# Kernel optimization log

Hardware: AMD Instinct MI355X
Metric: run time of the kernel (lower is better)

The kernel has to match this reference:

```python
import jax, jax.numpy as jnp
import numpy as np
from jax import lax

B_, L_, D_ = 4, 2048, 256
DI, NS, DC, DTR = 512, 16, 4, 16  # d_inner=2*D, d_state, d_conv, dt_rank=ceil(D/16)
DFF = 4 * D_


def setup_inputs():
    key = jax.random.key(0)
    ks = jax.random.split(key, 20)
    rn = lambda k, s, sc=0.02: jax.random.normal(k, s, jnp.float32) * sc
    return {
        "x": jax.random.normal(ks[0], (B_, L_, D_), jnp.float32),
        "in_proj_w": rn(ks[1], (2 * DI, D_)), "in_proj_b": jnp.zeros((2 * DI,), jnp.float32),
        "conv_w": rn(ks[2], (DI, DC), 0.1), "conv_b": jnp.zeros((DI,), jnp.float32),
        "x_proj_w": rn(ks[3], (DTR + 2 * NS, DI)),
        "dt_proj_w": rn(ks[4], (DI, DTR), 0.1), "dt_proj_b": rn(ks[5], (DI,), 0.5),
        "A_log": jnp.log(jnp.tile(jnp.arange(1, NS + 1, dtype=jnp.float32), (DI, 1))),
        "D_ssm": jnp.ones((DI,), jnp.float32),
        "out_proj_w": rn(ks[6], (D_, DI)), "out_proj_b": jnp.zeros((D_,), jnp.float32),
        "ln1_g": jnp.ones((D_,), jnp.float32), "ln1_b": jnp.zeros((D_,), jnp.float32),
        "fc1_w": rn(ks[7], (DFF, D_)), "fc1_b": jnp.zeros((DFF,), jnp.float32),
        "fc2_w": rn(ks[8], (D_, DFF)), "fc2_b": jnp.zeros((D_,), jnp.float32),
        "ln2_g": jnp.ones((D_,), jnp.float32), "ln2_b": jnp.zeros((D_,), jnp.float32),
    }


def _layer_norm(x, g, b, eps=1e-5):
    m = jnp.mean(x, -1, keepdims=True)
    v = jnp.mean((x - m) ** 2, -1, keepdims=True)
    return (x - m) / jnp.sqrt(v + eps) * g + b


def _mamba(x, in_proj_w, in_proj_b, conv_w, conv_b, x_proj_w, dt_proj_w, dt_proj_b, A_log, D_ssm, out_proj_w, out_proj_b):
    B, L, D = x.shape
    xz = x @ in_proj_w.T + in_proj_b                       # [B,L,2*DI]
    xi, z = jnp.split(xz, 2, axis=-1)
    # causal depthwise conv over time
    xc = jnp.transpose(xi, (0, 2, 1))                       # [B,DI,L]
    xc = lax.conv_general_dilated(xc, conv_w[:, None, :], (1,), [(DC - 1, 0)],
                                  dimension_numbers=("NCH", "OIH", "NCH"),
                                  feature_group_count=DI)
    xi = jax.nn.silu(jnp.transpose(xc + conv_b[None, :, None], (0, 2, 1)))  # [B,L,DI]
    x_dbl = xi @ x_proj_w.T                                 # [B,L,DTR+2*NS]
    dt, Bs, Cs = jnp.split(x_dbl, [DTR, DTR + NS], axis=-1)
    dt = jax.nn.softplus(dt @ dt_proj_w.T + dt_proj_b)      # [B,L,DI]
    A = -jnp.exp(A_log)                                     # [DI,NS]
    dA = jnp.exp(dt[..., None] * A)                         # [B,L,DI,NS]
    dBu = dt[..., None] * Bs[:, :, None, :] * xi[..., None]  # [B,L,DI,NS]
    dA_t = jnp.moveaxis(dA, 1, 0)
    dBu_t = jnp.moveaxis(dBu, 1, 0)
    C_t = jnp.moveaxis(Cs, 1, 0)                            # [L,B,NS]

    def step(h, inp):
        a, bu, c = inp
        h = a * h + bu                                      # [B,DI,NS]
        y = jnp.einsum("bdn,bn->bd", h, c)
        return h, y

    h0 = jnp.zeros((B, DI, NS), x.dtype)
    _, ys = lax.scan(step, h0, (dA_t, dBu_t, C_t))
    y = jnp.moveaxis(ys, 0, 1) + xi * D_ssm                 # [B,L,DI]
    y = y * jax.nn.silu(z)
    return y @ out_proj_w.T + out_proj_b


def reference(x, in_proj_w, in_proj_b, conv_w, conv_b, x_proj_w, dt_proj_w, dt_proj_b,
              A_log, D_ssm, out_proj_w, out_proj_b, ln1_g, ln1_b, fc1_w, fc1_b,
              fc2_w, fc2_b, ln2_g, ln2_b):
    gelu = lambda t: jax.nn.gelu(t, approximate=False)
    ssm = _mamba(x, in_proj_w, in_proj_b, conv_w, conv_b, x_proj_w, dt_proj_w,
                 dt_proj_b, A_log, D_ssm, out_proj_w, out_proj_b)
    y = _layer_norm(x + ssm, ln1_g, ln1_b)                  # dropout = identity (eval)
    ffn = gelu(gelu(y @ fc1_w.T + fc1_b) @ fc2_w.T + fc2_b)
    return _layer_norm(y + ffn, ln2_g, ln2_b)
```

## Files before the change

### kernel.cpp

```cpp
#include <hip/hip_runtime.h>

typedef __bf16 bf16x8 __attribute__((ext_vector_type(8)));
typedef float  f32x4  __attribute__((ext_vector_type(4)));

#define AS1 __attribute__((address_space(1)))
#define AS3 __attribute__((address_space(3)))

__device__ __forceinline__ float bf2f(ushort u) {
    union { unsigned int i; float f; } v; v.i = ((unsigned int)u) << 16; return v.f;
}
__device__ __forceinline__ ushort f2bf(float f) {
    union { float f; unsigned int i; } v; v.f = f;
    unsigned int i = v.i;
    unsigned int r = i + 0x7FFFu + ((i >> 16) & 1u);
    return (ushort)(r >> 16);
}
__device__ __forceinline__ float bflo(unsigned int u) { return bf2f((ushort)(u & 0xFFFFu)); }
__device__ __forceinline__ float bfhi(unsigned int u) { return bf2f((ushort)(u >> 16)); }
__device__ __forceinline__ float gelu_f(float v) {
    return 0.5f * v * (1.f + erff(v * 0.70710678118654752f));
}

__device__ __forceinline__ bool sniff_inline(const ushort* __restrict__ x) {
    const int lane = threadIdx.x & 63;
    int cnt = 0;
    #pragma unroll
    for (int r = 0; r < 4; r++) {
        const ushort u = x[lane + r * 64];
        const int e = (u >> 7) & 0xFF;
        if ((u & 0x7FFF) == 0 || (e >= 112 && e <= 141)) cnt++;
    }
    #pragma unroll
    for (int o = 32; o > 0; o >>= 1) cnt += __shfl_xor(cnt, o);
    return cnt >= 224;
}

struct CanonArgs {
    const void* src[20];
    int off[20];
    int total;
};

__launch_bounds__(256)
__global__ void canon_k(CanonArgs a, ushort* __restrict__ dst, ushort* __restrict__ xpw_pad,
                        const ushort* __restrict__ sniffx)
{
    const int i = blockIdx.x * 256 + threadIdx.x;
    if (i >= a.total) {
        const int j = i - a.total;
        if (j < 8192) xpw_pad[24576 + j] = 0;
        return;
    }
    const bool fl = sniff_inline(sniffx);
    int s = 0;
    #pragma unroll
    for (int t = 1; t < 20; t++) if (i >= a.off[t]) s = t;
    const int li = i - a.off[s];
    ushort v;
    if (fl) v = ((const ushort*)a.src[s])[li];
    else    v = f2bf(((const float*)a.src[s])[li]);
    dst[i] = v;
    if (s == 5) xpw_pad[li] = v;
}

template<int BM, int BN>
__launch_bounds__(256, 2)
__global__ void gemm_bt(const ushort* __restrict__ A, const ushort* __restrict__ W,
                        const ushort* __restrict__ bias, ushort* __restrict__ Cb,
                        int N, int K)
{
    constexpr int WMT = BM / 32;
    constexpr int WNT = BN / 32;
    __shared__ __align__(16) ushort As[BM * 32];
    __shared__ __align__(16) ushort Bs[BN * 32];
    const int tid  = threadIdx.x;
    const int wave = tid >> 6;
    const int lane = tid & 63;
    const int m0 = blockIdx.x * BM;
    const int n0 = blockIdx.y * BN;
    const int wm = (wave >> 1) * (BM / 2);
    const int wn = (wave & 1) * (BN / 2);
    const int lrow = lane & 15;
    const int quad = lane >> 4;

    f32x4 acc[WMT][WNT];
    #pragma unroll
    for (int i = 0; i < WMT; i++)
        #pragma unroll
        for (int j = 0; j < WNT; j++)
            #pragma unroll
            for (int r = 0; r < 4; r++) acc[i][j][r] = 0.f;

    for (int k0 = 0; k0 < K; k0 += 32) {
        #pragma unroll
        for (int t = 0; t < BM / 64; t++) {
            const int inst = t * 4 + wave;
            const int row  = inst * 16 + (lane >> 2);
            const int sub  = lane & 3;
            const ushort* gp = A + (size_t)(m0 + row) * K + (k0 + sub * 8);
            __builtin_amdgcn_global_load_lds((AS1 void*)(void*)gp,
                                             (AS3 void*)(As + inst * 512), 16, 0, 0);
        }
        #pragma unroll
        for (int t = 0; t < BN / 64; t++) {
            const int inst = t * 4 + wave;
            const int row  = inst * 16 + (lane >> 2);
            const int sub  = lane & 3;
            const ushort* gp = W + (size_t)(n0 + row) * K + (k0 + sub * 8);
            __builtin_amdgcn_global_load_lds((AS1 void*)(void*)gp,
                                             (AS3 void*)(Bs + inst * 512), 16, 0, 0);
        }
        __syncthreads();
        bf16x8 afr[WMT], bfr[WNT];
        #pragma unroll
        for (int i = 0; i < WMT; i++)
            afr[i] = *(const bf16x8*)&As[(wm + i * 16 + lrow) * 32 + quad * 8];
        #pragma unroll
        for (int j = 0; j < WNT; j++)
            bfr[j] = *(const bf16x8*)&Bs[(wn + j * 16 + lrow) * 32 + quad * 8];
        #pragma unroll
        for (int i = 0; i < WMT; i++)
            #pragma unroll
            for (int j = 0; j < WNT; j++)
                acc[i][j] = __builtin_amdgcn_mfma_f32_16x16x32_bf16(afr[i], bfr[j], acc[i][j], 0, 0, 0);
        __syncthreads();
    }

    #pragma unroll
    for (int i = 0; i < WMT; i++) {
        const int gm = m0 + wm + i * 16 + quad * 4;
        #pragma unroll
        for (int j = 0; j < WNT; j++) {
            const int gn = n0 + wn + j * 16 + lrow;
            const float bv = bf2f(bias[gn]);
            #pragma unroll
            for (int r = 0; r < 4; r++)
                Cb[(size_t)(gm + r) * N + gn] = f2bf(acc[i][j][r] + bv);
        }
    }
}

__launch_bounds__(512)
__global__ void convx_k(const ushort* __restrict__ xz, const ushort* __restrict__ cw,
                        const ushort* __restrict__ cb, const ushort* __restrict__ xpw_pad,
                        ushort* __restrict__ xc, float* __restrict__ xdbl)
{
    __shared__ __align__(16) ushort xcs[16 * 520];
    const int tid  = threadIdx.x;
    const int wave = tid >> 6;
    const int lane = tid & 63;
    const int lrow = lane & 15;
    const int quad = lane >> 4;
    const int c = blockIdx.x, b = blockIdx.y;
    const int t0 = b * 2048 + c * 16;

    {
        const int d8 = (tid & 63) * 8;
        ushort wl[32];
        *(uint4*)&wl[0]  = *(const uint4*)&cw[d8 * 4];
        *(uint4*)&wl[8]  = *(const uint4*)&cw[d8 * 4 + 8];
        *(uint4*)&wl[16] = *(const uint4*)&cw[d8 * 4 + 16];
        *(uint4*)&wl[24] = *(const uint4*)&cw[d8 * 4 + 24];
        ushort bl[8];
        *(uint4*)&bl[0] = *(const uint4*)&cb[d8];
        #pragma unroll
        for (int it = 0; it < 2; it++) {
            const int trow = it * 8 + wave;
            const int t = t0 + trow;
            const int l = t & 2047;
            float acc[8];
            #pragma unroll
            for (int j = 0; j < 8; j++) acc[j] = bf2f(bl[j]);
            #pragma unroll
            for (int k = 0; k < 4; k++) {
                const int ls = l - 3 + k;
                if (ls >= 0) {
                    ushort xl[8];
                    *(uint4*)&xl[0] = *(const uint4*)&xz[(size_t)(t - 3 + k) * 1024 + d8];
                    #pragma unroll
                    for (int j = 0; j < 8; j++) acc[j] += bf2f(xl[j]) * bf2f(wl[j * 4 + k]);
                }
            }
            ushort ol[8];
            #pragma unroll
            for (int j = 0; j < 8; j++) {
                const float s = acc[j] / (1.f + __expf(-acc[j]));
                ol[j] = f2bf(s);
            }
            *(uint4*)&xcs[trow * 520 + d8] = *(uint4*)&ol[0];
        }
    }
    __syncthreads();

    if (wave < 3) {
        const int nt = wave;
        const ushort* bptr = xpw_pad + (size_t)(nt * 16 + lrow) * 512 + quad * 8;
        f32x4 acc = {0.f, 0.f, 0.f, 0.f};
        #pragma unroll
        for (int hh = 0; hh < 2; hh++) {
            bf16x8 Bv[8];
            #pragma unroll
            for (int s = 0; s < 8; s++)
                Bv[s] = *(const bf16x8*)(bptr + hh * 256 + s * 32);
            #pragma unroll
            for (int s = 0; s < 8; s++) {
                const bf16x8 afr = *(const bf16x8*)&xcs[lrow * 520 + hh * 256 + s * 32 + quad * 8];
                acc = __builtin_amdgcn_mfma_f32_16x16x32_bf16(afr, Bv[s], acc, 0, 0, 0);
            }
        }
        const int col = nt * 16 + lrow;
        if (col < 48) {
            #pragma unroll
            for (int r = 0; r < 4; r++)
                xdbl[(size_t)(t0 + quad * 4 + r) * 64 + col] = acc[r];
        }
    }

    {
        const int row = tid >> 5;
        const int col = (tid & 31) * 16;
        *(uint4*)&xc[(size_t)(t0 + row) * 512 + col]     = *(const uint4*)&xcs[row * 520 + col];
        *(uint4*)&xc[(size_t)(t0 + row) * 512 + col + 8] = *(const uint4*)&xcs[row * 520 + col + 8];
    }
}

__launch_bounds__(256)
__global__ void scan1_k(const ushort* __restrict__ xc, const float* __restrict__ xdbl,
                        const ushort* __restrict__ dtw, const ushort* __restrict__ dtb,
                        const ushort* __restrict__ Alog,
                        float* __restrict__ summh, float* __restrict__ sdtb)
{
    __shared__ float XD[16 * 48];
    const int tid = threadIdx.x;
    const int c = blockIdx.x, dh = blockIdx.y, b = blockIdx.z;
    const int t0 = b * 2048 + c * 16;
    const int d = dh * 256 + tid;

    for (int e = tid; e < 768; e += 256)
        XD[e] = xdbl[(size_t)(t0 + (e / 48)) * 64 + (e % 48)];
    __syncthreads();

    const uint4 w0 = *(const uint4*)&dtw[d * 16];
    const uint4 w1 = *(const uint4*)&dtw[d * 16 + 8];
    const float wd[16] = { bflo(w0.x), bfhi(w0.x), bflo(w0.y), bfhi(w0.y),
                           bflo(w0.z), bfhi(w0.z), bflo(w0.w), bfhi(w0.w),
                           bflo(w1.x), bfhi(w1.x), bflo(w1.y), bfhi(w1.y),
                           bflo(w1.z), bfhi(w1.z), bflo(w1.w), bfhi(w1.w) };
    const uint4 a0 = *(const uint4*)&Alog[d * 16];
    const uint4 a1 = *(const uint4*)&Alog[d * 16 + 8];
    const float al[16] = { bflo(a0.x), bfhi(a0.x), bflo(a0.y), bfhi(a0.y),
                           bflo(a0.z), bfhi(a0.z), bflo(a0.w), bfhi(a0.w),
                           bflo(a1.x), bfhi(a1.x), bflo(a1.y), bfhi(a1.y),
                           bflo(a1.z), bfhi(a1.z), bflo(a1.w), bfhi(a1.w) };
    const float dtbv = bf2f(dtb[d]);
    float A[16], h[16];
    #pragma unroll
    for (int n = 0; n < 16; n++) { A[n] = -__expf(al[n]); h[n] = 0.f; }
    float sdt = 0.f;
    for (int i = 0; i < 16; i++) {
        const float* Xr = &XD[i * 48];
        float s0 = dtbv, s1 = 0.f, s2 = 0.f, s3 = 0.f;
        #pragma unroll
        for (int k = 0; k < 16; k += 4) {
            s0 += Xr[k]     * wd[k];
            s1 += Xr[k + 1] * wd[k + 1];
            s2 += Xr[k + 2] * wd[k + 2];
            s3 += Xr[k + 3] * wd[k + 3];
        }
        const float s = (s0 + s1) + (s2 + s3);
        const float dtv = (s > 15.f) ? s : __logf(1.f + __expf(s));
        const float xiv = bf2f(xc[(size_t)(t0 + i) * 512 + d]);
        const float dx = dtv * xiv;
        sdt += dtv;
        #pragma unroll
        for (int n = 0; n < 16; n++) {
            const float da = __expf(dtv * A[n]);
            h[n] = da * h[n] + dx * Xr[16 + n];
        }
    }
    const size_t bh = ((size_t)(b * 128 + c) * 16) * 512 + d;
    #pragma unroll
    for (int n = 0; n < 16; n++) summh[bh + (size_t)n * 512] = h[n];
    sdtb[(size_t)(b * 128 + c) * 512 + d] = sdt;
}

__launch_bounds__(128)
__global__ void combine_k(float* __restrict__ summh, const float* __restrict__ sdtb,
                          const ushort* __restrict__ Alog)
{
    const int b  = blockIdx.x >> 6;
    const int n  = (blockIdx.x >> 2) & 15;
    const int dq = blockIdx.x & 3;
    const int d  = dq * 128 + threadIdx.x;
    const float An = -__expf(bf2f(Alog[d * 16 + n]));
    float h = 0.f;
    #pragma unroll
    for (int q = 0; q < 4; q++) {
        float p[32], hl[32], ho[32];
        #pragma unroll
        for (int c2 = 0; c2 < 32; c2++) {
            const int cc = q * 32 + c2;
            hl[c2] = summh[((size_t)(b * 128 + cc) * 16 + n) * 512 + d];
            p[c2]  = __expf(An * sdtb[(size_t)(b * 128 + cc) * 512 + d]);
        }
        #pragma unroll
        for (int c2 = 0; c2 < 32; c2++) {
            ho[c2] = h;
            h = p[c2] * h + hl[c2];
        }
        #pragma unroll
        for (int c2 = 0; c2 < 32; c2++)
            summh[((size_t)(b * 128 + (q * 32 + c2)) * 16 + n) * 512 + d] = ho[c2];
    }
}

__launch_bounds__(256)
__global__ void scan2_k(ushort* __restrict__ xz, const ushort* __restrict__ xc,
                        const float* __restrict__ xdbl,
                        const ushort* __restrict__ dtw, const ushort* __restrict__ dtb,
                        const ushort* __restrict__ Alog, const float* __restrict__ summh,
                        const ushort* __restrict__ Dssm)
{
    __shared__ float XD[16 * 48];
    const int tid = threadIdx.x;
    const int c = blockIdx.x, dh = blockIdx.y, b = blockIdx.z;
    const int t0 = b * 2048 + c * 16;
    const int d = dh * 256 + tid;

    for (int e = tid; e < 768; e += 256)
        XD[e] = xdbl[(size_t)(t0 + (e / 48)) * 64 + (e % 48)];
    __syncthreads();

    const uint4 w0 = *(const uint4*)&dtw[d * 16];
    const uint4 w1 = *(const uint4*)&dtw[d * 16 + 8];
    const float wd[16] = { bflo(w0.x), bfhi(w0.x), bflo(w0.y), bfhi(w0.y),
                           bflo(w0.z), bfhi(w0.z), bflo(w0.w), bfhi(w0.w),
                           bflo(w1.x), bfhi(w1.x), bflo(w1.y), bfhi(w1.y),
                           bflo(w1.z), bfhi(w1.z), bflo(w1.w), bfhi(w1.w) };
    const uint4 a0 = *(const uint4*)&Alog[d * 16];
    const uint4 a1 = *(const uint4*)&Alog[d * 16 + 8];
    const float al[16] = { bflo(a0.x), bfhi(a0.x), bflo(a0.y), bfhi(a0.y),
                           bflo(a0.z), bfhi(a0.z), bflo(a0.w), bfhi(a0.w),
                           bflo(a1.x), bfhi(a1.x), bflo(a1.y), bfhi(a1.y),
                           bflo(a1.z), bfhi(a1.z), bflo(a1.w), bfhi(a1.w) };
    const float dtbv = bf2f(dtb[d]);
    float A[16], h[16];
    #pragma unroll
    for (int n = 0; n < 16; n++) A[n] = -__expf(al[n]);
    const size_t bh = ((size_t)(b * 128 + c) * 16) * 512 + d;
    #pragma unroll
    for (int n = 0; n < 16; n++) h[n] = summh[bh + (size_t)n * 512];
    const float Dv = bf2f(Dssm[d]);

    for (int i = 0; i < 16; i++) {
        const int t = t0 + i;
        const float* Xr = &XD[i * 48];
        float s0 = dtbv, s1 = 0.f, s2 = 0.f, s3 = 0.f;
        #pragma unroll
        for (int k = 0; k < 16; k += 4) {
            s0 += Xr[k]     * wd[k];
            s1 += Xr[k + 1] * wd[k + 1];
            s2 += Xr[k + 2] * wd[k + 2];
            s3 += Xr[k + 3] * wd[k + 3];
        }
        const float s = (s0 + s1) + (s2 + s3);
        const float dtv = (s > 15.f) ? s : __logf(1.f + __expf(s));
        const float xiv = bf2f(xc[(size_t)t * 512 + d]);
        const float dx = dtv * xiv;
        float yv0 = 0.f, yv1 = 0.f;
        #pragma unroll
        for (int n = 0; n < 16; n += 2) {
            const float da0 = __expf(dtv * A[n]);
            const float da1 = __expf(dtv * A[n + 1]);
            h[n]     = da0 * h[n]     + dx * Xr[16 + n];
            h[n + 1] = da1 * h[n + 1] + dx * Xr[17 + n];
            yv0 += h[n]     * Xr[32 + n];
            yv1 += h[n + 1] * Xr[33 + n];
        }
        float yv = yv0 + yv1;
        yv += xiv * Dv;
        const float zv = bf2f(xz[(size_t)t * 1024 + 512 + d]);
        yv *= zv / (1.f + __expf(-zv));
        xz[(size_t)t * 1024 + d] = f2bf(yv);
    }
}

__launch_bounds__(512, 4)
__global__ void ffn_k(const ushort* __restrict__ xz, const ushort* __restrict__ cx,
                      const ushort* __restrict__ opw, const ushort* __restrict__ opb,
                      const ushort* __restrict__ ln1g, const ushort* __restrict__ ln1b,
                      const ushort* __restrict__ f1w, const ushort* __restrict__ f1b,
                      const ushort* __restrict__ f2w, const ushort* __restrict__ f2b,
                      const ushort* __restrict__ ln2g, const ushort* __restrict__ ln2b,
                      void* __restrict__ dout, const ushort* __restrict__ sniffx)
{
    __shared__ __align__(16) ushort yls[16 * 520];
    __shared__ __align__(16) ushort y1bs[16 * 264];
    __shared__ float redS[8 * 16], redQ[8 * 16];
    ushort* f1q = yls;

    const int tid  = threadIdx.x;
    const int wave = tid >> 6;
    const int lane = tid & 63;
    const int lrow = lane & 15;
    const int quad = lane >> 4;
    const int c = blockIdx.x, b = blockIdx.y;
    const int t0 = b * 2048 + c * 16;
    const int n0w = wave * 32;

    {
        const int row = tid >> 5;
        const int col = (tid & 31) * 16;
        *(uint4*)&yls[row * 520 + col]     = *(const uint4*)&xz[(size_t)(t0 + row) * 1024 + col];
        *(uint4*)&yls[row * 520 + col + 8] = *(const uint4*)&xz[(size_t)(t0 + row) * 1024 + col + 8];
    }
    __syncthreads();

    f32x4 accP[2];
    #pragma unroll
    for (int j = 0; j < 2; j++)
        #pragma unroll
        for (int r = 0; r < 4; r++) accP[j][r] = 0.f;
    {
        const ushort* bp0 = opw + (size_t)(n0w + lrow) * 512 + quad * 8;
        const ushort* bp1 = opw + (size_t)(n0w + 16 + lrow) * 512 + quad * 8;
        #pragma unroll
        for (int hh = 0; hh < 2; hh++) {
            bf16x8 B0[8], B1[8];
            #pragma unroll
            for (int s = 0; s < 8; s++) {
                B0[s] = *(const bf16x8*)(bp0 + hh * 256 + s * 32);
                B1[s] = *(const bf16x8*)(bp1 + hh * 256 + s * 32);
            }
            #pragma unroll
            for (int s = 0; s < 8; s++) {
                const bf16x8 afr = *(const bf16x8*)&yls[lrow * 520 + hh * 256 + s * 32 + quad * 8];
                accP[0] = __builtin_amdgcn_mfma_f32_16x16x32_bf16(afr, B0[s], accP[0], 0, 0, 0);
                accP[1] = __builtin_amdgcn_mfma_f32_16x16x32_bf16(afr, B1[s], accP[1], 0, 0, 0);
            }
        }
    }
    float vP[2][4];
    float ps[4], pq[4];
    #pragma unroll
    for (int r = 0; r < 4; r++) { ps[r] = 0.f; pq[r] = 0.f; }
    #pragma unroll
    for (int j = 0; j < 2; j++) {
        const int col = n0w + j * 16 + lrow;
        const float bv = bf2f(opb[col]);
        #pragma unroll
        for (int r = 0; r < 4; r++) {
            const int row = quad * 4 + r;
            float v = accP[j][r] + bv + bf2f(cx[(size_t)(t0 + row) * 256 + col]);
            vP[j][r] = v;
            ps[r] += v;
            pq[r] += v * v;
        }
    }
    #pragma unroll
    for (int r = 0; r < 4; r++) {
        #pragma unroll
        for (int o = 8; o > 0; o >>= 1) {
            ps[r] += __shfl_xor(ps[r], o);
            pq[r] += __shfl_xor(pq[r], o);
        }
        if (lrow == 0) {
            const int row = quad * 4 + r;
            redS[wave * 16 + row] = ps[r];
            redQ[wave * 16 + row] = pq[r];
        }
    }
    __syncthreads();

    float y1f[2][4];
    #pragma unroll
    for (int r = 0; r < 4; r++) {
        const int row = quad * 4 + r;
        float S = 0.f, Q = 0.f;
        #pragma unroll
        for (int w = 0; w < 8; w++) { S += redS[w * 16 + row]; Q += redQ[w * 16 + row]; }
        const float mean = S * (1.f / 256.f);
        const float var  = Q * (1.f / 256.f) - mean * mean;
        const float rs   = rsqrtf(var + 1e-5f);
        #pragma unroll
        for (int j = 0; j < 2; j++) {
            const int col = n0w + j * 16 + lrow;
            const float o2 = (vP[j][r] - mean) * rs * bf2f(ln1g[col]) + bf2f(ln1b[col]);
            y1f[j][r] = o2;
            y1bs[row * 264 + col] = f2bf(o2);
        }
    }
    __syncthreads();

    f32x4 acc2[2];
    #pragma unroll
    for (int j = 0; j < 2; j++)
        #pragma unroll
        for (int r = 0; r < 4; r++) acc2[j][r] = 0.f;

    for (int q = 0; q < 4; q++) {
        f32x4 a1[2];
        #pragma unroll
        for (int j = 0; j < 2; j++)
            #pragma unroll
            for (int r = 0; r < 4; r++) a1[j][r] = 0.f;
        {
            const ushort* bp0 = f1w + (size_t)(q * 256 + n0w + lrow) * 256 + quad * 8;
            const ushort* bp1 = f1w + (size_t)(q * 256 + n0w + 16 + lrow) * 256 + quad * 8;
            bf16x8 B0[8], B1[8];
            #pragma unroll
            for (int s = 0; s < 8; s++) {
                B0[s] = *(const bf16x8*)(bp0 + s * 32);
                B1[s] = *(const bf16x8*)(bp1 + s * 32);
            }
            #pragma unroll
            for (int s = 0; s < 8; s++) {
                const bf16x8 afr = *(const bf16x8*)&y1bs[lrow * 264 + s * 32 + quad * 8];
                a1[0] = __builtin_amdgcn_mfma_f32_16x16x32_bf16(afr, B0[s], a1[0], 0, 0, 0);
                a1[1] = __builtin_amdgcn_mfma_f32_16x16x32_bf16(afr, B1[s], a1[1], 0, 0, 0);
            }
        }
        #pragma unroll
        for (int j = 0; j < 2; j++) {
            const int qc = n0w + j * 16 + lrow;
            const float bv = bf2f(f1b[q * 256 + qc]);
            #pragma unroll
            for (int r = 0; r < 4; r++) {
                const int row = quad * 4 + r;
                f1q[row * 260 + qc] = f2bf(gelu_f(a1[j][r] + bv));
            }
        }
        __syncthreads();
        {
            const ushort* bp0 = f2w + (size_t)(n0w + lrow) * 1024 + q * 256 + quad * 8;
            const ushort* bp1 = f2w + (size_t)(n0w + 16 + lrow) * 1024 + q * 256 + quad * 8;
            bf16x8 B0[8], B1[8];
            #pragma unroll
            for (int s = 0; s < 8; s++) {
                B0[s] = *(const bf16x8*)(bp0 + s * 32);
                B1[s] = *(const bf16x8*)(bp1 + s * 32);
            }
            #pragma unroll
            for (int s = 0; s < 8; s++) {
                const bf16x8 afr = *(const bf16x8*)&f1q[lrow * 260 + s * 32 + quad * 8];
                acc2[0] = __builtin_amdgcn_mfma_f32_16x16x32_bf16(afr, B0[s], acc2[0], 0, 0, 0);
                acc2[1] = __builtin_amdgcn_mfma_f32_16x16x32_bf16(afr, B1[s], acc2[1], 0, 0, 0);
            }
        }
        __syncthreads();
    }

    float v2[2][4];
    #pragma unroll
    for (int r = 0; r < 4; r++) { ps[r] = 0.f; pq[r] = 0.f; }
    #pragma unroll
    for (int j = 0; j < 2; j++) {
        const int col = n0w + j * 16 + lrow;
        const float bv = bf2f(f2b[col]);
        #pragma unroll
        for (int r = 0; r < 4; r++) {
            const float v = gelu_f(acc2[j][r] + bv) + y1f[j][r];
            v2[j][r] = v;
            ps[r] += v;
            pq[r] += v * v;
        }
    }
    #pragma unroll
    for (int r = 0; r < 4; r++) {
        #pragma unroll
        for (int o = 8; o > 0; o >>= 1) {
            ps[r] += __shfl_xor(ps[r], o);
            pq[r] += __shfl_xor(pq[r], o);
        }
        if (lrow == 0) {
            const int row = quad * 4 + r;
            redS[wave * 16 + row] = ps[r];
            redQ[wave * 16 + row] = pq[r];
        }
    }
    __syncthreads();

    const bool fl = sniff_inline(sniffx);
    #pragma unroll
    for (int r = 0; r < 4; r++) {
        const int row = quad * 4 + r;
        float S = 0.f, Q = 0.f;
        #pragma unroll
        for (int w = 0; w < 8; w++) { S += redS[w * 16 + row]; Q += redQ[w * 16 + row]; }
        const float mean = S * (1.f / 256.f);
        const float var  = Q * (1.f / 256.f) - mean * mean;
        const float rs   = rsqrtf(var + 1e-5f);
        #pragma unroll
        for (int j = 0; j < 2; j++) {
            const int col = n0w + j * 16 + lrow;
            const size_t off = (size_t)(t0 + row) * 256 + col;
            const float o2 = (v2[j][r] - mean) * rs * bf2f(ln2g[col]) + bf2f(ln2b[col]);
            if (fl) ((ushort*)dout)[off] = f2bf(o2);
            else    ((float*)dout)[off]  = o2;
        }
    }
}

extern "C" void kernel_launch(void* const* d_in, const int* in_sizes, int n_in,
                              void* d_out, int out_size, void* d_ws, size_t ws_size,
                              hipStream_t stream)
{
    char* ws = (char*)d_ws;
    ushort* canon = (ushort*)(ws + 256);

    static const int coff[20] = {
        0,        2097152,  2359296,  2360320,  2362368,
        2362880,  2387456,  2395648,  2396160,  2404352,
        2404864,  2535936,  2536192,  2536448,  2536704,
        2798848,  2799872,  3062016,  3062272,  3062528 };
    static const int ctot = 3062784;

    CanonArgs ca;
    for (int i = 0; i < 20; i++) { ca.src[i] = d_in[i]; ca.off[i] = coff[i]; }
    ca.total = ctot;

    const ushort* cx   = canon + coff[0];
    const ushort* cipw = canon + coff[1];
    const ushort* cipb = canon + coff[2];
    const ushort* ccw  = canon + coff[3];
    const ushort* ccb  = canon + coff[4];
    const ushort* cdtw = canon + coff[6];
    const ushort* cdtb = canon + coff[7];
    const ushort* calog= canon + coff[8];
    const ushort* cdssm= canon + coff[9];
    const ushort* copw = canon + coff[10];
    const ushort* copb = canon + coff[11];
    const ushort* cln1g= canon + coff[12];
    const ushort* cln1b= canon + coff[13];
    const ushort* cf1w = canon + coff[14];
    const ushort* cf1b = canon + coff[15];
    const ushort* cf2w = canon + coff[16];
    const ushort* cf2b = canon + coff[17];
    const ushort* cln2g= canon + coff[18];
    const ushort* cln2b= canon + coff[19];

    ushort* xpw_pad = (ushort*)(ws + 6291456);
    ushort* xz      = (ushort*)(ws + 8388608);
    float*  xdbl    = (float*)(ws + 25165824);
    float*  summh   = (float*)(ws + 27262976);
    float*  sdtb    = (float*)(ws + 44040192);
    ushort* xc      = (ushort*)(ws + 45088768);
    const ushort* sx = (const ushort*)d_in[0];

    canon_k<<<(ctot + 8192 + 255) / 256, 256, 0, stream>>>(ca, canon, xpw_pad, sx);
    gemm_bt<128, 128><<<dim3(64, 8), 256, 0, stream>>>(cx, cipw, cipb, xz, 1024, 256);
    convx_k<<<dim3(128, 4), 512, 0, stream>>>(xz, ccw, ccb, xpw_pad, xc, xdbl);
    scan1_k<<<dim3(128, 2, 4), 256, 0, stream>>>(xc, xdbl, cdtw, cdtb, calog, summh, sdtb);
    combine_k<<<256, 128, 0, stream>>>(summh, sdtb, calog);
    scan2_k<<<dim3(128, 2, 4), 256, 0, stream>>>(xz, xc, xdbl, cdtw, cdtb, calog, summh, cdssm);
    ffn_k<<<dim3(128, 4), 512, 0, stream>>>(
        xz, cx, copw, copb, cln1g, cln1b, cf1w, cf1b, cf2w, cf2b, cln2g, cln2b,
        d_out, sx);
}
```

Measured before the change: 274.0 us.

## Split fused FFN kernel into tiled GEMMs with LN1 and LN2 epilogue kernels

Replaces the monolithic per-16-row ffn_k, which reloaded weights from global per block, with a 128x256 out_proj GEMM fused with residual plus LayerNorm1, two tiled LDS GEMMs for fc1 (with GELU epilogue) and fc2 (fp32 output), and a small LN2 kernel. The aim is better weight reuse and MFMA utilisation through larger tiles. The cost is extra kernel launches and global round-trips for y1, h1 and y2, plus reuse of workspace regions. scan2 now writes its output into xc instead of xz.

New measurement: 278.2 us. About the same (+1.5%).

```diff
diff --git a/kernel.cpp b/kernel.cpp
--- a/kernel.cpp
+++ b/kernel.cpp
@@ -63,10 +63,10 @@
     if (s == 5) xpw_pad[li] = v;
 }
 
-template<int BM, int BN>
+template<int BM, int BN, int EPI, bool OUTF>
 __launch_bounds__(256, 2)
-__global__ void gemm_bt(const ushort* __restrict__ A, const ushort* __restrict__ W,
-                        const ushort* __restrict__ bias, ushort* __restrict__ Cb,
+__global__ void gemm_bt(const ushort* __restrict__ A, int lda, const ushort* __restrict__ W,
+                        const ushort* __restrict__ bias, void* __restrict__ Cb,
                         int N, int K)
 {
     constexpr int WMT = BM / 32;
@@ -97,7 +97,7 @@
             const int inst = t * 4 + wave;
             const int row  = inst * 16 + (lane >> 2);
             const int sub  = lane & 3;
-            const ushort* gp = A + (size_t)(m0 + row) * K + (k0 + sub * 8);
+            const ushort* gp = A + (size_t)(m0 + row) * lda + (k0 + sub * 8);
             __builtin_amdgcn_global_load_lds((AS1 void*)(void*)gp,
                                              (AS3 void*)(As + inst * 512), 16, 0, 0);
         }
@@ -134,8 +134,130 @@
             const int gn = n0 + wn + j * 16 + lrow;
             const float bv = bf2f(bias[gn]);
             #pragma unroll
-            for (int r = 0; r < 4; r++)
-                Cb[(size_t)(gm + r) * N + gn] = f2bf(acc[i][j][r] + bv);
+            for (int r = 0; r < 4; r++) {
+                float v = acc[i][j][r] + bv;
+                if (EPI == 1) v = gelu_f(v);
+                if (OUTF) ((float*)Cb)[(size_t)(gm + r) * N + gn] = v;
+                else      ((ushort*)Cb)[(size_t)(gm + r) * N + gn] = f2bf(v);
+            }
+        }
+    }
+}
+
+__launch_bounds__(512)
+__global__ void gemmln1_k(const ushort* __restrict__ A, const ushort* __restrict__ W,
+                          const ushort* __restrict__ bias, const ushort* __restrict__ cx,
+                          const ushort* __restrict__ g1, const ushort* __restrict__ b1,
+                          ushort* __restrict__ y1b, float* __restrict__ y1f)
+{
+    __shared__ __align__(16) ushort As[128 * 32];
+    __shared__ __align__(16) ushort Bs[256 * 32];
+    __shared__ float redS[4 * 128], redQ[4 * 128];
+    const int tid  = threadIdx.x;
+    const int wave = tid >> 6;
+    const int lane = tid & 63;
+    const int lrow = lane & 15;
+    const int quad = lane >> 4;
+    const int m0 = blockIdx.x * 128;
+    const int wm = (wave >> 2) * 64;
+    const int wn = (wave & 3) * 64;
+
+    f32x4 acc[4][4];
+    #pragma unroll
+    for (int i = 0; i < 4; i++)
+        #pragma unroll
+        for (int j = 0; j < 4; j++)
+            #pragma unroll
+            for (int r = 0; r < 4; r++) acc[i][j][r] = 0.f;
+
+    for (int k0 = 0; k0 < 512; k0 += 32) {
+        {
+            const int row = wave * 16 + (lane >> 2);
+            const int sub = lane & 3;
+            const ushort* gp = A + (size_t)(m0 + row) * 512 + (k0 + sub * 8);
+            __builtin_amdgcn_global_load_lds((AS1 void*)(void*)gp,
+                                             (AS3 void*)(As + wave * 512), 16, 0, 0);
+        }
+        #pragma unroll
+        for (int t = 0; t < 2; t++) {
+            const int inst = t * 8 + wave;
+            const int row  = inst * 16 + (lane >> 2);
+            const int sub  = lane & 3;
+            const ushort* gp = W + (size_t)row * 512 + (k0 + sub * 8);
+            __builtin_amdgcn_global_load_lds((AS1 void*)(void*)gp,
+                                             (AS3 void*)(Bs + inst * 512), 16, 0, 0);
+        }
+        __syncthreads();
+        bf16x8 afr[4], bfr[4];
+        #pragma unroll
+        for (int i = 0; i < 4; i++)
+            afr[i] = *(const bf16x8*)&As[(wm + i * 16 + lrow) * 32 + quad * 8];
+        #pragma unroll
+        for (int j = 0; j < 4; j++)
+            bfr[j] = *(const bf16x8*)&Bs[(wn + j * 16 + lrow) * 32 + quad * 8];
+        #pragma unroll
+        for (int i = 0; i < 4; i++)
+            #pragma unroll
+            for (int j = 0; j < 4; j++)
+                acc[i][j] = __builtin_amdgcn_mfma_f32_16x16x32_bf16(afr[i], bfr[j], acc[i][j], 0, 0, 0);
+        __syncthreads();
+    }
+
+    #pragma unroll
+    for (int i = 0; i < 4; i++) {
+        #pragma unroll
+        for (int j = 0; j < 4; j++) {
+            const int col = wn + j * 16 + lrow;
+            const float bv = bf2f(bias[col]);
+            #pragma unroll
+            for (int r = 0; r < 4; r++) {
+                const int rowl = wm + i * 16 + quad * 4 + r;
+                acc[i][j][r] += bv + bf2f(cx[(size_t)(m0 + rowl) * 256 + col]);
+            }
+        }
+    }
+    #pragma unroll
+    for (int i = 0; i < 4; i++) {
+        #pragma unroll
+        for (int r = 0; r < 4; r++) {
+            float s = 0.f, q = 0.f;
+            #pragma unroll
+            for (int j = 0; j < 4; j++) {
+                const float v = acc[i][j][r];
+                s += v; q += v * v;
+            }
+            #pragma unroll
+            for (int o = 8; o > 0; o >>= 1) {
+                s += __shfl_xor(s, o);
+                q += __shfl_xor(q, o);
+            }
+            if (lrow == 0) {
+                const int rowl = wm + i * 16 + quad * 4 + r;
+                redS[(wave & 3) * 128 + rowl] = s;
+                redQ[(wave & 3) * 128 + rowl] = q;
+            }
+        }
+    }
+    __syncthreads();
+
+    #pragma unroll
+    for (int i = 0; i < 4; i++) {
+        #pragma unroll
+        for (int r = 0; r < 4; r++) {
+            const int rowl = wm + i * 16 + quad * 4 + r;
+            const float S = redS[rowl] + redS[128 + rowl] + redS[256 + rowl] + redS[384 + rowl];
+            const float Q = redQ[rowl] + redQ[128 + rowl] + redQ[256 + rowl] + redQ[384 + rowl];
+            const float mean = S * (1.f / 256.f);
+            const float var  = Q * (1.f / 256.f) - mean * mean;
+            const float rs   = rsqrtf(var + 1e-5f);
+            #pragma unroll
+            for (int j = 0; j < 4; j++) {
+                const int col = wn + j * 16 + lrow;
+                const float o2 = (acc[i][j][r] - mean) * rs * bf2f(g1[col]) + bf2f(b1[col]);
+                const size_t off = (size_t)(m0 + rowl) * 256 + col;
+                y1b[off] = f2bf(o2);
+                y1f[off] = o2;
+            }
         }
     }
 }
@@ -315,7 +437,7 @@
 }
 
 __launch_bounds__(256)
-__global__ void scan2_k(ushort* __restrict__ xz, const ushort* __restrict__ xc,
+__global__ void scan2_k(const ushort* __restrict__ xz, ushort* __restrict__ xc,
                         const float* __restrict__ xdbl,
                         const ushort* __restrict__ dtw, const ushort* __restrict__ dtb,
                         const ushort* __restrict__ Alog, const float* __restrict__ summh,
@@ -381,223 +503,53 @@
         yv += xiv * Dv;
         const float zv = bf2f(xz[(size_t)t * 1024 + 512 + d]);
         yv *= zv / (1.f + __expf(-zv));
-        xz[(size_t)t * 1024 + d] = f2bf(yv);
-    }
-}
-
-__launch_bounds__(512, 4)
-__global__ void ffn_k(const ushort* __restrict__ xz, const ushort* __restrict__ cx,
-                      const ushort* __restrict__ opw, const ushort* __restrict__ opb,
-                      const ushort* __restrict__ ln1g, const ushort* __restrict__ ln1b,
-                      const ushort* __restrict__ f1w, const ushort* __restrict__ f1b,
-                      const ushort* __restrict__ f2w, const ushort* __restrict__ f2b,
-                      const ushort* __restrict__ ln2g, const ushort* __restrict__ ln2b,
+        xc[(size_t)t * 512 + d] = f2bf(yv);
+    }
+}
+
+__launch_bounds__(512)
+__global__ void ln2_k(const float* __restrict__ y2, const float* __restrict__ y1f,
+                      const ushort* __restrict__ g2, const ushort* __restrict__ b2,
                       void* __restrict__ dout, const ushort* __restrict__ sniffx)
 {
-    __shared__ __align__(16) ushort yls[16 * 520];
-    __shared__ __align__(16) ushort y1bs[16 * 264];
-    __shared__ float redS[8 * 16], redQ[8 * 16];
-    ushort* f1q = yls;
-
     const int tid  = threadIdx.x;
     const int wave = tid >> 6;
     const int lane = tid & 63;
-    const int lrow = lane & 15;
-    const int quad = lane >> 4;
-    const int c = blockIdx.x, b = blockIdx.y;
-    const int t0 = b * 2048 + c * 16;
-    const int n0w = wave * 32;
-
-    {
-        const int row = tid >> 5;
-        const int col = (tid & 31) * 16;
-        *(uint4*)&yls[row * 520 + col]     = *(const uint4*)&xz[(size_t)(t0 + row) * 1024 + col];
-        *(uint4*)&yls[row * 520 + col + 8] = *(const uint4*)&xz[(size_t)(t0 + row) * 1024 + col + 8];
-    }
-    __syncthreads();
-
-    f32x4 accP[2];
-    #pragma unroll
-    for (int j = 0; j < 2; j++)
-        #pragma unroll
-        for (int r = 0; r < 4; r++) accP[j][r] = 0.f;
-    {
-        const ushort* bp0 = opw + (size_t)(n0w + lrow) * 512 + quad * 8;
-        const ushort* bp1 = opw + (size_t)(n0w + 16 + lrow) * 512 + quad * 8;
-        #pragma unroll
-        for (int hh = 0; hh < 2; hh++) {
-            bf16x8 B0[8], B1[8];
-            #pragma unroll
-            for (int s = 0; s < 8; s++) {
-                B0[s] = *(const bf16x8*)(bp0 + hh * 256 + s * 32);
-                B1[s] = *(const bf16x8*)(bp1 + hh * 256 + s * 32);
-            }
-            #pragma unroll
-            for (int s = 0; s < 8; s++) {
-                const bf16x8 afr = *(const bf16x8*)&yls[lrow * 520 + hh * 256 + s * 32 + quad * 8];
-                accP[0] = __builtin_amdgcn_mfma_f32_16x16x32_bf16(afr, B0[s], accP[0], 0, 0, 0);
-                accP[1] = __builtin_amdgcn_mfma_f32_16x16x32_bf16(afr, B1[s], accP[1], 0, 0, 0);
-            }
-        }
-    }
-    float vP[2][4];
-    float ps[4], pq[4];
-    #pragma unroll
-    for (int r = 0; r < 4; r++) { ps[r] = 0.f; pq[r] = 0.f; }
-    #pragma unroll
-    for (int j = 0; j < 2; j++) {
-        const int col = n0w + j * 16 + lrow;
-        const float bv = bf2f(opb[col]);
-        #pragma unroll
-        for (int r = 0; r < 4; r++) {
-            const int row = quad * 4 + r;
-            float v = accP[j][r] + bv + bf2f(cx[(size_t)(t0 + row) * 256 + col]);
-            vP[j][r] = v;
-            ps[r] += v;
-            pq[r] += v * v;
-        }
-    }
-    #pragma unroll
-    for (int r = 0; r < 4; r++) {
-        #pragma unroll
-        for (int o = 8; o > 0; o >>= 1) {
-            ps[r] += __shfl_xor(ps[r], o);
-            pq[r] += __shfl_xor(pq[r], o);
-        }
-        if (lrow == 0) {
-            const int row = quad * 4 + r;
-            redS[wave * 16 + row] = ps[r];
-            redQ[wave * 16 + row] = pq[r];
-        }
-    }
-    __syncthreads();
-
-    float y1f[2][4];
-    #pragma unroll
-    for (int r = 0; r < 4; r++) {
-        const int row = quad * 4 + r;
-        float S = 0.f, Q = 0.f;
-        #pragma unroll
-        for (int w = 0; w < 8; w++) { S += redS[w * 16 + row]; Q += redQ[w * 16 + row]; }
-        const float mean = S * (1.f / 256.f);
-        const float var  = Q * (1.f / 256.f) - mean * mean;
-        const float rs   = rsqrtf(var + 1e-5f);
-        #pragma unroll
-        for (int j = 0; j < 2; j++) {
-            const int col = n0w + j * 16 + lrow;
-            const float o2 = (vP[j][r] - mean) * rs * bf2f(ln1g[col]) + bf2f(ln1b[col]);
-            y1f[j][r] = o2;
-            y1bs[row * 264 + col] = f2bf(o2);
-        }
-    }
-    __syncthreads();
-
-    f32x4 acc2[2];
-    #pragma unroll
-    for (int j = 0; j < 2; j++)
-        #pragma unroll
-        for (int r = 0; r < 4; r++) acc2[j][r] = 0.f;
-
-    for (int q = 0; q < 4; q++) {
-        f32x4 a1[2];
-        #pragma unroll
-        for (int j = 0; j < 2; j++)
-            #pragma unroll
-            for (int r = 0; r < 4; r++) a1[j][r] = 0.f;
-        {
-            const ushort* bp0 = f1w + (size_t)(q * 256 + n0w + lrow) * 256 + quad * 8;
-            const ushort* bp1 = f1w + (size_t)(q * 256 + n0w + 16 + lrow) * 256 + quad * 8;
-            bf16x8 B0[8], B1[8];
-            #pragma unroll
-            for (int s = 0; s < 8; s++) {
-                B0[s] = *(const bf16x8*)(bp0 + s * 32);
-                B1[s] = *(const bf16x8*)(bp1 + s * 32);
-            }
-            #pragma unroll
-            for (int s = 0; s < 8; s++) {
-                const bf16x8 afr = *(const bf16x8*)&y1bs[lrow * 264 + s * 32 + quad * 8];
-                a1[0] = __builtin_amdgcn_mfma_f32_16x16x32_bf16(afr, B0[s], a1[0], 0, 0, 0);
-                a1[1] = __builtin_amdgcn_mfma_f32_16x16x32_bf16(afr, B1[s], a1[1], 0, 0, 0);
-            }
-        }
-        #pragma unroll
-        for (int j = 0; j < 2; j++) {
-            const int qc = n0w + j * 16 + lrow;
-            const float bv = bf2f(f1b[q * 256 + qc]);
-            #pragma unroll
-            for (int r = 0; r < 4; r++) {
-                const int row = quad * 4 + r;
-                f1q[row * 260 + qc] = f2bf(gelu_f(a1[j][r] + bv));
-            }
-        }
-        __syncthreads();
-        {
-            const ushort* bp0 = f2w + (size_t)(n0w + lrow) * 1024 + q * 256 + quad * 8;
-            const ushort* bp1 = f2w + (size_t)(n0w + 16 + lrow) * 1024 + q * 256 + quad * 8;
-            bf16x8 B0[8], B1[8];
-            #pragma unroll
-            for (int s = 0; s < 8; s++) {
-                B0[s] = *(const bf16x8*)(bp0 + s * 32);
-                B1[s] = *(const bf16x8*)(bp1 + s * 32);
-            }
-            #pragma unroll
-            for (int s = 0; s < 8; s++) {
-                const bf16x8 afr = *(const bf16x8*)&f1q[lrow * 260 + s * 32 + quad * 8];
-                acc2[0] = __builtin_amdgcn_mfma_f32_16x16x32_bf16(afr, B0[s], acc2[0], 0, 0, 0);
-                acc2[1] = __builtin_amdgcn_mfma_f32_16x16x32_bf16(afr, B1[s], acc2[1], 0, 0, 0);
-            }
-        }
-        __syncthreads();
-    }
-
-    float v2[2][4];
-    #pragma unroll
-    for (int r = 0; r < 4; r++) { ps[r] = 0.f; pq[r] = 0.f; }
-    #pragma unroll
-    for (int j = 0; j < 2; j++) {
-        const int col = n0w + j * 16 + lrow;
-        const float bv = bf2f(f2b[col]);
-        #pragma unroll
-        for (int r = 0; r < 4; r++) {
-            const float v = gelu_f(acc2[j][r] + bv) + y1f[j][r];
-            v2[j][r] = v;
-            ps[r] += v;
-            pq[r] += v * v;
-        }
-    }
-    #pragma unroll
-    for (int r = 0; r < 4; r++) {
-        #pragma unroll
-        for (int o = 8; o > 0; o >>= 1) {
-            ps[r] += __shfl_xor(ps[r], o);
-            pq[r] += __shfl_xor(pq[r], o);
-        }
-        if (lrow == 0) {
-            const int row = quad * 4 + r;
-            redS[wave * 16 + row] = ps[r];
-            redQ[wave * 16 + row] = pq[r];
-        }
-    }
-    __syncthreads();
+    const int row  = blockIdx.x * 8 + wave;
+    const int col0 = lane * 4;
+
+    const f32x4 a = *(const f32x4*)&y2[(size_t)row * 256 + col0];
+    const f32x4 rsd = *(const f32x4*)&y1f[(size_t)row * 256 + col0];
+    float v[4];
+    float S = 0.f, Q = 0.f;
+    #pragma unroll
+    for (int k = 0; k < 4; k++) {
+        v[k] = gelu_f(a[k]) + rsd[k];
+        S += v[k];
+        Q += v[k] * v[k];
+    }
+    #pragma unroll
+    for (int o = 32; o > 0; o >>= 1) {
+        S += __shfl_xor(S, o);
+        Q += __shfl_xor(Q, o);
+    }
+    const float mean = S * (1.f / 256.f);
+    const float var  = Q * (1.f / 256.f) - mean * mean;
+    const float rs   = rsqrtf(var + 1e-5f);
 
     const bool fl = sniff_inline(sniffx);
-    #pragma unroll
-    for (int r = 0; r < 4; r++) {
-        const int row = quad * 4 + r;
-        float S = 0.f, Q = 0.f;
-        #pragma unroll
-        for (int w = 0; w < 8; w++) { S += redS[w * 16 + row]; Q += redQ[w * 16 + row]; }
-        const float mean = S * (1.f / 256.f);
-        const float var  = Q * (1.f / 256.f) - mean * mean;
-        const float rs   = rsqrtf(var + 1e-5f);
-        #pragma unroll
-        for (int j = 0; j < 2; j++) {
-            const int col = n0w + j * 16 + lrow;
-            const size_t off = (size_t)(t0 + row) * 256 + col;
-            const float o2 = (v2[j][r] - mean) * rs * bf2f(ln2g[col]) + bf2f(ln2b[col]);
-            if (fl) ((ushort*)dout)[off] = f2bf(o2);
-            else    ((float*)dout)[off]  = o2;
-        }
+    if (fl) {
+        ushort o4[4];
+        #pragma unroll
+        for (int k = 0; k < 4; k++)
+            o4[k] = f2bf((v[k] - mean) * rs * bf2f(g2[col0 + k]) + bf2f(b2[col0 + k]));
+        *(ushort4*)((ushort*)dout + (size_t)row * 256 + col0) = *(ushort4*)&o4[0];
+    } else {
+        float o4[4];
+        #pragma unroll
+        for (int k = 0; k < 4; k++)
+            o4[k] = (v[k] - mean) * rs * bf2f(g2[col0 + k]) + bf2f(b2[col0 + k]);
+        *(float4*)((float*)dout + (size_t)row * 256 + col0) = *(float4*)&o4[0];
     }
 }
 
@@ -641,19 +593,27 @@
 
     ushort* xpw_pad = (ushort*)(ws + 6291456);
     ushort* xz      = (ushort*)(ws + 8388608);
+    ushort* y1b     = (ushort*)(ws + 8388608);
+    float*  y1f     = (float*)(ws + 12582912);
     float*  xdbl    = (float*)(ws + 25165824);
     float*  summh   = (float*)(ws + 27262976);
+    ushort* h1      = (ushort*)(ws + 27262976);
     float*  sdtb    = (float*)(ws + 44040192);
     ushort* xc      = (ushort*)(ws + 45088768);
+    float*  y2      = (float*)(ws + 45088768);
     const ushort* sx = (const ushort*)d_in[0];
 
     canon_k<<<(ctot + 8192 + 255) / 256, 256, 0, stream>>>(ca, canon, xpw_pad, sx);
-    gemm_bt<128, 128><<<dim3(64, 8), 256, 0, stream>>>(cx, cipw, cipb, xz, 1024, 256);
+    gemm_bt<128, 128, 0, false><<<dim3(64, 8), 256, 0, stream>>>(
+        cx, 256, cipw, cipb, xz, 1024, 256);
     convx_k<<<dim3(128, 4), 512, 0, stream>>>(xz, ccw, ccb, xpw_pad, xc, xdbl);
     scan1_k<<<dim3(128, 2, 4), 256, 0, stream>>>(xc, xdbl, cdtw, cdtb, calog, summh, sdtb);
     combine_k<<<256, 128, 0, stream>>>(summh, sdtb, calog);
     scan2_k<<<dim3(128, 2, 4), 256, 0, stream>>>(xz, xc, xdbl, cdtw, cdtb, calog, summh, cdssm);
-    ffn_k<<<dim3(128, 4), 512, 0, stream>>>(
-        xz, cx, copw, copb, cln1g, cln1b, cf1w, cf1b, cf2w, cf2b, cln2g, cln2b,
-        d_out, sx);
-}
+    gemmln1_k<<<64, 512, 0, stream>>>(xc, copw, copb, cx, cln1g, cln1b, y1b, y1f);
+    gemm_bt<128, 128, 1, false><<<dim3(64, 8), 256, 0, stream>>>(
+        y1b, 256, cf1w, cf1b, h1, 1024, 256);
+    gemm_bt<128, 128, 0, true><<<dim3(64, 2), 256, 0, stream>>>(
+        h1, 1024, cf2w, cf2b, y2, 256, 1024);
+    ln2_k<<<1024, 512, 0, stream>>>(y2, y1f, cln2g, cln2b, d_out, sx);
+}
```
